# Kernel tuning notes

Measured on AMD Instinct MI355X. Metric: run time of the kernel, lower is better.

The kernel has to match this reference:

```python
import jax, jax.numpy as jnp
import numpy as np
import math

N_HEAD = 16  # from init_kwargs

def setup_inputs() -> dict:
    key = jax.random.key(0)
    ks = jax.random.split(key, 11)
    B, T, D = 2, 2048, 1024
    s = 0.02
    return {
        "q": jax.random.normal(ks[0], (B, T, D), jnp.float32),
        "k": jax.random.normal(ks[1], (B, T, D), jnp.float32),
        "v": jax.random.normal(ks[2], (B, T, D), jnp.float32),
        "Wq": jax.random.normal(ks[3], (D, D), jnp.float32) * s,
        "bq": jax.random.normal(ks[4], (D,), jnp.float32) * s,
        "Wk": jax.random.normal(ks[5], (D, D), jnp.float32) * s,
        "bk": jax.random.normal(ks[6], (D,), jnp.float32) * s,
        "Wv": jax.random.normal(ks[7], (D, D), jnp.float32) * s,
        "bv": jax.random.normal(ks[8], (D,), jnp.float32) * s,
        "Wc": jax.random.normal(ks[9], (D, D), jnp.float32) * s,
        "bc": jax.random.normal(ks[10], (D,), jnp.float32) * s,
    }

def reference(q, k, v, Wq, bq, Wk, bk, Wv, bv, Wc, bc):
    B, T, D = q.shape
    H = N_HEAD
    nd = D // H

    def proj(x, W, b):
        # torch Linear: x @ W.T + b; then split heads -> [b, h, t, nd]
        y = x @ W.T + b
        return y.reshape(B, T, H, nd).transpose(0, 2, 1, 3)

    qh = proj(q, Wq, bq)
    kh = proj(k, Wk, bk)
    vh = proj(v, Wv, bv)

    # scores: [b, h, t_q, t_k]
    z = jnp.einsum('bhqd,bhkd->bhqk', qh, kh) / math.sqrt(nd)
    mask = jnp.tril(jnp.ones((T, T), dtype=bool))  # causal
    z = jnp.where(mask, z, -jnp.inf)
    # NOTE: original uses nn.Softmax(dim=-2) -> softmax over the QUERY axis
    attn = jax.nn.softmax(z, axis=-2)
    out = jnp.einsum('bhqk,bhkd->bhqd', attn, vh)  # [b, h, t, nd]
    out = out.transpose(0, 2, 1, 3).reshape(B, T, D)
    return out @ Wc.T + bc
```

## Files before the change

kernel.cpp:

```cpp
#include <hip/hip_runtime.h>


#define Dd 1024
#define Tt 2048
#define Bb 2
#define Hh 16
#define NDh 64
#define Mm (Bb * Tt)

using u16 = unsigned short;
using u32 = unsigned int;
typedef __attribute__((ext_vector_type(8))) short bf16x8;
typedef __attribute__((ext_vector_type(4))) float f32x4;

__device__ __forceinline__ u16 f2bf(float f) {
  return (u16)((__float_as_uint(f) + 0x8000u) >> 16);
}
__device__ __forceinline__ u32 pk2(float a, float b) {
  u32 ua = __float_as_uint(a) + 0x8000u;
  u32 ub = __float_as_uint(b) + 0x8000u;
  return __builtin_amdgcn_perm(ub, ua, 0x07060302u);
}
__device__ __forceinline__ void ldsdma16(const u16* g, u16* l) {
  __builtin_amdgcn_global_load_lds(
      (const __attribute__((address_space(1))) u32*)g,
      (__attribute__((address_space(3))) u32*)l, 16, 0, 0);
}
#define MFMA(a, b, c) __builtin_amdgcn_mfma_f32_16x16x32_bf16((a), (b), (c), 0, 0, 0)

__global__ __launch_bounds__(256) void cvt_w(
    const float* __restrict__ w0, const float* __restrict__ w1,
    const float* __restrict__ w2, const float* __restrict__ w3,
    u16* __restrict__ dst)
{
  const int vid = blockIdx.x * 256 + threadIdx.x;
  const int seg = vid >> 18;
  const int off = (vid & 0x3FFFF) * 4;
  const float* s = seg == 0 ? w0 : seg == 1 ? w1 : seg == 2 ? w2 : w3;
  float4 f = *(const float4*)(s + off);
  ushort4 o;
  o.x = f2bf(f.x); o.y = f2bf(f.y); o.z = f2bf(f.z); o.w = f2bf(f.w);
  *(ushort4*)(dst + (size_t)seg * Dd * Dd + off) = o;
}

template <bool XF32>
__device__ __forceinline__ void gemm_body(
    const void* Xv, const u16* __restrict__ WB, const float* __restrict__ bias,
    void* Yv, float oscale, int omode, u16* As, u16* Bs)
{
  const int t = threadIdx.x, lane = t & 63, w = t >> 6;
  const int col = lane & 15, quad = lane >> 4;
  const int m0 = blockIdx.x * 64, n0 = blockIdx.y * 128;
  const int wm = (w >> 1) * 32, wn = (w & 1) * 64;
  const int drr = lane >> 3, dcc = (lane & 7) * 8;
  const int ar = t >> 2, ac = (t & 3) * 16;

  f32x4 acc[2][4] = {};
  float4 xf[4];
  const float* X32 = (const float*)Xv;
  if constexpr (XF32) {
#pragma unroll
    for (int j = 0; j < 4; j++)
      xf[j] = ((const float4*)(X32 + (size_t)(m0 + ar) * Dd + ac))[j];
  }

  for (int k0 = 0; k0 < Dd; k0 += 64) {
    __syncthreads();
#pragma unroll
    for (int i = 0; i < 4; i++) {
      const int rr = w * 32 + i * 8;
      ldsdma16(WB + (size_t)(n0 + rr + drr) * Dd + k0 + dcc, Bs + rr * 64);
    }
    if constexpr (XF32) {
      u32 pk[8];
#pragma unroll
      for (int j = 0; j < 4; j++) {
        pk[2 * j]     = pk2(xf[j].x, xf[j].y);
        pk[2 * j + 1] = pk2(xf[j].z, xf[j].w);
      }
      u16* dst = As + ar * 64 + ac;
      ((uint4*)dst)[0] = make_uint4(pk[0], pk[1], pk[2], pk[3]);
      ((uint4*)dst)[1] = make_uint4(pk[4], pk[5], pk[6], pk[7]);
      if (k0 + 64 < Dd) {
#pragma unroll
        for (int j = 0; j < 4; j++)
          xf[j] = ((const float4*)(X32 + (size_t)(m0 + ar) * Dd + k0 + 64 + ac))[j];
      }
    } else {
      const u16* X = (const u16*)Xv;
#pragma unroll
      for (int i = 0; i < 2; i++) {
        const int rr = w * 16 + i * 8;
        ldsdma16(X + (size_t)(m0 + rr + drr) * Dd + k0 + dcc, As + rr * 64);
      }
    }
    __syncthreads();
#pragma unroll
    for (int s = 0; s < 2; s++) {
      bf16x8 a[2], b[4];
#pragma unroll
      for (int i = 0; i < 2; i++)
        a[i] = *(const bf16x8*)(As + (wm + i * 16 + col) * 64 + s * 32 + quad * 8);
#pragma unroll
      for (int j = 0; j < 4; j++)
        b[j] = *(const bf16x8*)(Bs + (wn + j * 16 + col) * 64 + s * 32 + quad * 8);
#pragma unroll
      for (int i = 0; i < 2; i++)
#pragma unroll
        for (int j = 0; j < 4; j++)
          acc[i][j] = MFMA(a[i], b[j], acc[i][j]);
    }
  }

#pragma unroll
  for (int jt = 0; jt < 4; jt++) {
    const int n = n0 + wn + jt * 16 + col;
    const float bn = bias[n];
    if (omode == 1) {
#pragma unroll
      for (int i = 0; i < 2; i++) {
        const int mg = m0 + wm + i * 16 + quad * 4;
        const int bb = mg >> 11, tl = mg & 2047;
        ushort4 o;
        o.x = f2bf(acc[i][jt][0] + bn);
        o.y = f2bf(acc[i][jt][1] + bn);
        o.z = f2bf(acc[i][jt][2] + bn);
        o.w = f2bf(acc[i][jt][3] + bn);
        *(ushort4*)((u16*)Yv + (size_t)bb * Dd * Tt + (size_t)n * Tt + tl) = o;
      }
    } else if (omode == 0) {
      u16* Y = (u16*)Yv;
#pragma unroll
      for (int i = 0; i < 2; i++)
#pragma unroll
        for (int r = 0; r < 4; r++) {
          const int m = m0 + wm + i * 16 + quad * 4 + r;
          Y[(size_t)m * Dd + n] = f2bf((acc[i][jt][r] + bn) * oscale);
        }
    } else {
      float* Y = (float*)Yv;
#pragma unroll
      for (int i = 0; i < 2; i++)
#pragma unroll
        for (int r = 0; r < 4; r++) {
          const int m = m0 + wm + i * 16 + quad * 4 + r;
          Y[(size_t)m * Dd + n] = acc[i][jt][r] + bn;
        }
    }
  }
}

__global__ __launch_bounds__(256) void proj_qkv(
    const float* __restrict__ q, const float* __restrict__ k,
    const float* __restrict__ v, const u16* __restrict__ Wb,
    const float* __restrict__ bq, const float* __restrict__ bk,
    const float* __restrict__ bv,
    u16* __restrict__ Qp, u16* __restrict__ Kp, u16* __restrict__ VtG)
{
  __shared__ u16 As[64 * 64];
  __shared__ u16 Bs[128 * 64];
  const int z = blockIdx.z;
  const float* X = z == 0 ? q : z == 1 ? k : v;
  const u16* W = Wb + (size_t)z * Dd * Dd;
  const float* bias = z == 0 ? bq : z == 1 ? bk : bv;
  void* Y = z == 0 ? (void*)Qp : z == 1 ? (void*)Kp : (void*)VtG;
  gemm_body<true>(X, W, bias, Y, z == 0 ? 0.125f : 1.0f, z == 2 ? 1 : 0, As, Bs);
}

__global__ __launch_bounds__(256) void gemm_final(
    const u16* __restrict__ Ctx, const u16* __restrict__ Wcb,
    const float* __restrict__ bc, float* __restrict__ out)
{
  __shared__ u16 As[64 * 64];
  __shared__ u16 Bs[128 * 64];
  gemm_body<false>(Ctx, Wcb, bc, out, 1.0f, 2, As, Bs);
}

__global__ __launch_bounds__(256) void attn_stats(
    const u16* __restrict__ Qp, const u16* __restrict__ Kp,
    float* __restrict__ rlOut)
{
  __shared__ u16 Ks[128 * 64];
  __shared__ u16 Qs[64 * 64];
  const int t = threadIdx.x, lane = t & 63, w = t >> 6;
  const int col = lane & 15, quad = lane >> 4;
  const int bh = blockIdx.x, b = bh >> 4, h = bh & 15;
  const int tk0 = blockIdx.y * 128;
  const u16* Kbase = Kp + (size_t)b * Tt * Dd + h * NDh;
  const u16* Qbase = Qp + (size_t)b * Tt * Dd + h * NDh;
  const int drr = lane >> 3, dcc = (lane & 7) * 8;

#pragma unroll
  for (int i = 0; i < 4; i++) {
    const int rr = w * 32 + i * 8;
    ldsdma16(Kbase + (size_t)(tk0 + rr + drr) * Dd + dcc, Ks + rr * 64);
  }
  __syncthreads();
  bf16x8 ka[2][2];
#pragma unroll
  for (int s2 = 0; s2 < 2; s2++) {
    const int row = w * 32 + s2 * 16 + col;
    ka[s2][0] = *(const bf16x8*)(Ks + row * 64 + quad * 8);
    ka[s2][1] = *(const bf16x8*)(Ks + row * 64 + 32 + quad * 8);
  }

  float l[2][4] = {};

  auto tile = [&](int tq0, bool masked) {
    __syncthreads();
#pragma unroll
    for (int i = 0; i < 2; i++) {
      const int rr = w * 16 + i * 8;
      ldsdma16(Qbase + (size_t)(tq0 + rr + drr) * Dd + dcc, Qs + rr * 64);
    }
    __syncthreads();
#pragma unroll
    for (int jt = 0; jt < 4; jt++) {
      bf16x8 qb0 = *(const bf16x8*)(Qs + (jt * 16 + col) * 64 + quad * 8);
      bf16x8 qb1 = *(const bf16x8*)(Qs + (jt * 16 + col) * 64 + 32 + quad * 8);
      const int tq = tq0 + jt * 16 + col;
#pragma unroll
      for (int s2 = 0; s2 < 2; s2++) {
        f32x4 z = {};
        z = MFMA(ka[s2][0], qb0, z);
        z = MFMA(ka[s2][1], qb1, z);
#pragma unroll
        for (int r = 0; r < 4; r++) {
          float e = __expf(z[r]);
          if (masked) {
            const int tk = tk0 + w * 32 + s2 * 16 + quad * 4 + r;
            e = (tq >= tk) ? e : 0.f;
          }
          l[s2][r] += e;
        }
      }
    }
  };

  tile(tk0, true);
  tile(tk0 + 64, true);
  for (int tq0 = tk0 + 128; tq0 < Tt; tq0 += 64) tile(tq0, false);

#pragma unroll
  for (int s2 = 0; s2 < 2; s2++)
#pragma unroll
    for (int r = 0; r < 4; r++) {
      float s = l[s2][r];
#pragma unroll
      for (int m = 1; m < 16; m <<= 1) s += __shfl_xor(s, m);
      if (col == 0)
        rlOut[(size_t)bh * Tt + tk0 + w * 32 + s2 * 16 + quad * 4 + r] = 1.0f / s;
    }
}

__global__ __launch_bounds__(256) void attn_out(
    const u16* __restrict__ Qp, const u16* __restrict__ Kp,
    const u16* __restrict__ VtG, const float* __restrict__ rlIn,
    u16* __restrict__ Ctx)
{
  __shared__ u16 PQ[128 * 64];
  __shared__ u16 Ks[64 * 64];
  __shared__ u16 Vts[64 * 64];
  __shared__ float srl[64];
  const int t = threadIdx.x, lane = t & 63, w = t >> 6;
  const int col = lane & 15, quad = lane >> 4;
  const int bh = blockIdx.x, b = bh >> 4, h = bh & 15;
  const int tq0 = blockIdx.y * 128;
  const u16* Qbase = Qp + (size_t)b * Tt * Dd + h * NDh;
  const u16* Kbase = Kp + (size_t)b * Tt * Dd + h * NDh;
  const u16* Vbase = VtG + (size_t)b * Dd * Tt + (size_t)h * NDh * Tt;
  const int drr = lane >> 3, dcc = (lane & 7) * 8;

#pragma unroll
  for (int i = 0; i < 4; i++) {
    const int rr = w * 32 + i * 8;
    ldsdma16(Qbase + (size_t)(tq0 + rr + drr) * Dd + dcc, PQ + rr * 64);
  }
  __syncthreads();
  bf16x8 qa[2][2];
#pragma unroll
  for (int s2 = 0; s2 < 2; s2++) {
    const int row = w * 32 + s2 * 16 + col;
    qa[s2][0] = *(const bf16x8*)(PQ + row * 64 + quad * 8);
    qa[s2][1] = *(const bf16x8*)(PQ + row * 64 + 32 + quad * 8);
  }

  f32x4 o[2][4] = {};

  auto tile = [&](int tk0, bool masked) {
    __syncthreads();
#pragma unroll
    for (int i = 0; i < 2; i++) {
      const int rr = w * 16 + i * 8;
      ldsdma16(Kbase + (size_t)(tk0 + rr + drr) * Dd + dcc, Ks + rr * 64);
      ldsdma16(Vbase + (size_t)(rr + drr) * Tt + tk0 + dcc, Vts + rr * 64);
    }
    if (t < 64) srl[t] = rlIn[(size_t)bh * Tt + tk0 + t];
    __syncthreads();
#pragma unroll
    for (int jt = 0; jt < 4; jt++) {
      bf16x8 kb0 = *(const bf16x8*)(Ks + (jt * 16 + col) * 64 + quad * 8);
      bf16x8 kb1 = *(const bf16x8*)(Ks + (jt * 16 + col) * 64 + 32 + quad * 8);
      const int tkl = jt * 16 + col;
      const float rl = srl[tkl];
#pragma unroll
      for (int s2 = 0; s2 < 2; s2++) {
        f32x4 z = {};
        z = MFMA(qa[s2][0], kb0, z);
        z = MFMA(qa[s2][1], kb1, z);
#pragma unroll
        for (int r = 0; r < 4; r++) {
          float p = __expf(z[r]) * rl;
          if (masked) {
            const int tqg = tq0 + w * 32 + s2 * 16 + quad * 4 + r;
            p = (tk0 + tkl <= tqg) ? p : 0.f;
          }
          PQ[(w * 32 + s2 * 16 + quad * 4 + r) * 64 + tkl] = f2bf(p);
        }
      }
    }
    bf16x8 pa[2][2];
#pragma unroll
    for (int s2 = 0; s2 < 2; s2++) {
      const int row = w * 32 + s2 * 16 + col;
      pa[s2][0] = *(const bf16x8*)(PQ + row * 64 + quad * 8);
      pa[s2][1] = *(const bf16x8*)(PQ + row * 64 + 32 + quad * 8);
    }
#pragma unroll
    for (int dn = 0; dn < 4; dn++) {
      bf16x8 vb0 = *(const bf16x8*)(Vts + (dn * 16 + col) * 64 + quad * 8);
      bf16x8 vb1 = *(const bf16x8*)(Vts + (dn * 16 + col) * 64 + 32 + quad * 8);
#pragma unroll
      for (int s2 = 0; s2 < 2; s2++) {
        o[s2][dn] = MFMA(pa[s2][0], vb0, o[s2][dn]);
        o[s2][dn] = MFMA(pa[s2][1], vb1, o[s2][dn]);
      }
    }
  };

  for (int tk0 = 0; tk0 + 64 <= tq0; tk0 += 64) tile(tk0, false);
  tile(tq0, true);
  tile(tq0 + 64, true);

#pragma unroll
  for (int s2 = 0; s2 < 2; s2++)
#pragma unroll
    for (int dn = 0; dn < 4; dn++)
#pragma unroll
      for (int r = 0; r < 4; r++) {
        const int tq = tq0 + w * 32 + s2 * 16 + quad * 4 + r;
        Ctx[(size_t)(b * Tt + tq) * Dd + h * NDh + dn * 16 + col] = f2bf(o[s2][dn][r]);
      }
}

extern "C" void kernel_launch(void* const* d_in, const int* in_sizes, int n_in,
                              void* d_out, int out_size, void* d_ws, size_t ws_size,
                              hipStream_t stream)
{
  const float* q  = (const float*)d_in[0];
  const float* k  = (const float*)d_in[1];
  const float* v  = (const float*)d_in[2];
  const float* Wq = (const float*)d_in[3];
  const float* bq = (const float*)d_in[4];
  const float* Wk = (const float*)d_in[5];
  const float* bk = (const float*)d_in[6];
  const float* Wv = (const float*)d_in[7];
  const float* bv = (const float*)d_in[8];
  const float* Wc = (const float*)d_in[9];
  const float* bc = (const float*)d_in[10];

  u16* Wb  = (u16*)d_ws;
  u16* Qp  = Wb + (size_t)4 * Dd * Dd;
  u16* Kp  = Qp + (size_t)Mm * Dd;
  u16* VtG = Kp + (size_t)Mm * Dd;
  u16* Ctx = VtG + (size_t)Mm * Dd;
  float* rl = (float*)(Ctx + (size_t)Mm * Dd);

  cvt_w<<<4096, 256, 0, stream>>>(Wq, Wk, Wv, Wc, Wb);
  proj_qkv<<<dim3(Mm / 64, Dd / 128, 3), 256, 0, stream>>>(
      q, k, v, Wb, bq, bk, bv, Qp, Kp, VtG);
  attn_stats<<<dim3(Bb * Hh, Tt / 128), 256, 0, stream>>>(Qp, Kp, rl);
  attn_out<<<dim3(Bb * Hh, Tt / 128), 256, 0, stream>>>(Qp, Kp, VtG, rl, Ctx);
  gemm_final<<<dim3(Mm / 64, Dd / 128), 256, 0, stream>>>(
      Ctx, Wb + (size_t)3 * Dd * Dd, bc, (float*)d_out);
}
```

Before: 279.1 us.

## Swizzle LDS tiles, split attention stats and final GEMM with atomics, finer attn_out blocks

Applies an XOR swizzle to all LDS tile layouts to reduce bank conflicts on MFMA fragment reads. attn_stats is split four ways along the query axis and accumulates column sums with atomics. attn_out moves to 64-row query blocks scheduled heaviest-first to balance the causal workload. The final GEMM is split-K across two slices with atomic float adds into an output zeroed in cvt_w. Together these raise parallelism and occupancy, at the cost of atomic traffic and non-deterministic summation order.

```diff
diff --git a/kernel.cpp b/kernel.cpp
--- a/kernel.cpp
+++ b/kernel.cpp
@@ -27,11 +27,14 @@
       (__attribute__((address_space(3))) u32*)l, 16, 0, 0);
 }
 #define MFMA(a, b, c) __builtin_amdgcn_mfma_f32_16x16x32_bf16((a), (b), (c), 0, 0, 0)
+__device__ __forceinline__ bf16x8 ldfrag(const u16* lds, int row, int kgrp) {
+  return *(const bf16x8*)(lds + row * 64 + (((kgrp) ^ (row & 7)) * 8));
+}
 
 __global__ __launch_bounds__(256) void cvt_w(
     const float* __restrict__ w0, const float* __restrict__ w1,
     const float* __restrict__ w2, const float* __restrict__ w3,
-    u16* __restrict__ dst)
+    u16* __restrict__ dst, float* __restrict__ outz, float* __restrict__ lsumz)
 {
   const int vid = blockIdx.x * 256 + threadIdx.x;
   const int seg = vid >> 18;
@@ -41,19 +44,23 @@
   ushort4 o;
   o.x = f2bf(f.x); o.y = f2bf(f.y); o.z = f2bf(f.z); o.w = f2bf(f.w);
   *(ushort4*)(dst + (size_t)seg * Dd * Dd + off) = o;
+  *(float4*)(outz + (size_t)vid * 4) = make_float4(0.f, 0.f, 0.f, 0.f);
+  if (vid < Bb * Hh * Tt / 4)
+    *(float4*)(lsumz + (size_t)vid * 4) = make_float4(0.f, 0.f, 0.f, 0.f);
 }
 
 template <bool XF32>
 __device__ __forceinline__ void gemm_body(
     const void* Xv, const u16* __restrict__ WB, const float* __restrict__ bias,
-    void* Yv, float oscale, int omode, u16* As, u16* Bs)
+    void* Yv, float oscale, int omode, int kc, int knum, u16* As, u16* Bs)
 {
   const int t = threadIdx.x, lane = t & 63, w = t >> 6;
   const int col = lane & 15, quad = lane >> 4;
   const int m0 = blockIdx.x * 64, n0 = blockIdx.y * 128;
   const int wm = (w >> 1) * 32, wn = (w & 1) * 64;
-  const int drr = lane >> 3, dcc = (lane & 7) * 8;
-  const int ar = t >> 2, ac = (t & 3) * 16;
+  const int drr = lane >> 3, dsw = ((lane & 7) ^ drr) * 8;
+  const int ar = t >> 2, ag = (t & 3) * 2;
+  const int kbeg = (Dd / knum) * kc, kend = kbeg + Dd / knum;
 
   f32x4 acc[2][4] = {};
   float4 xf[4];
@@ -61,15 +68,15 @@
   if constexpr (XF32) {
 #pragma unroll
     for (int j = 0; j < 4; j++)
-      xf[j] = ((const float4*)(X32 + (size_t)(m0 + ar) * Dd + ac))[j];
-  }
-
-  for (int k0 = 0; k0 < Dd; k0 += 64) {
+      xf[j] = ((const float4*)(X32 + (size_t)(m0 + ar) * Dd + kbeg + ag * 8))[j];
+  }
+
+  for (int k0 = kbeg; k0 < kend; k0 += 64) {
     __syncthreads();
 #pragma unroll
     for (int i = 0; i < 4; i++) {
       const int rr = w * 32 + i * 8;
-      ldsdma16(WB + (size_t)(n0 + rr + drr) * Dd + k0 + dcc, Bs + rr * 64);
+      ldsdma16(WB + (size_t)(n0 + rr + drr) * Dd + k0 + dsw, Bs + rr * 64);
     }
     if constexpr (XF32) {
       u32 pk[8];
@@ -78,20 +85,20 @@
         pk[2 * j]     = pk2(xf[j].x, xf[j].y);
         pk[2 * j + 1] = pk2(xf[j].z, xf[j].w);
       }
-      u16* dst = As + ar * 64 + ac;
-      ((uint4*)dst)[0] = make_uint4(pk[0], pk[1], pk[2], pk[3]);
-      ((uint4*)dst)[1] = make_uint4(pk[4], pk[5], pk[6], pk[7]);
-      if (k0 + 64 < Dd) {
+      u16* dst = As + ar * 64;
+      *(uint4*)(dst + ((ag ^ (ar & 7)) * 8))       = make_uint4(pk[0], pk[1], pk[2], pk[3]);
+      *(uint4*)(dst + (((ag + 1) ^ (ar & 7)) * 8)) = make_uint4(pk[4], pk[5], pk[6], pk[7]);
+      if (k0 + 64 < kend) {
 #pragma unroll
         for (int j = 0; j < 4; j++)
-          xf[j] = ((const float4*)(X32 + (size_t)(m0 + ar) * Dd + k0 + 64 + ac))[j];
+          xf[j] = ((const float4*)(X32 + (size_t)(m0 + ar) * Dd + k0 + 64 + ag * 8))[j];
       }
     } else {
       const u16* X = (const u16*)Xv;
 #pragma unroll
       for (int i = 0; i < 2; i++) {
         const int rr = w * 16 + i * 8;
-        ldsdma16(X + (size_t)(m0 + rr + drr) * Dd + k0 + dcc, As + rr * 64);
+        ldsdma16(X + (size_t)(m0 + rr + drr) * Dd + k0 + dsw, As + rr * 64);
       }
     }
     __syncthreads();
@@ -100,10 +107,10 @@
       bf16x8 a[2], b[4];
 #pragma unroll
       for (int i = 0; i < 2; i++)
-        a[i] = *(const bf16x8*)(As + (wm + i * 16 + col) * 64 + s * 32 + quad * 8);
+        a[i] = ldfrag(As, wm + i * 16 + col, s * 4 + quad);
 #pragma unroll
       for (int j = 0; j < 4; j++)
-        b[j] = *(const bf16x8*)(Bs + (wn + j * 16 + col) * 64 + s * 32 + quad * 8);
+        b[j] = ldfrag(Bs, wn + j * 16 + col, s * 4 + quad);
 #pragma unroll
       for (int i = 0; i < 2; i++)
 #pragma unroll
@@ -115,7 +122,7 @@
 #pragma unroll
   for (int jt = 0; jt < 4; jt++) {
     const int n = n0 + wn + jt * 16 + col;
-    const float bn = bias[n];
+    const float bn = (omode == 2 && kc != 0) ? 0.f : bias[n];
     if (omode == 1) {
 #pragma unroll
       for (int i = 0; i < 2; i++) {
@@ -144,7 +151,7 @@
 #pragma unroll
         for (int r = 0; r < 4; r++) {
           const int m = m0 + wm + i * 16 + quad * 4 + r;
-          Y[(size_t)m * Dd + n] = acc[i][jt][r] + bn;
+          atomicAdd(&Y[(size_t)m * Dd + n], acc[i][jt][r] + bn);
         }
     }
   }
@@ -164,7 +171,7 @@
   const u16* W = Wb + (size_t)z * Dd * Dd;
   const float* bias = z == 0 ? bq : z == 1 ? bk : bv;
   void* Y = z == 0 ? (void*)Qp : z == 1 ? (void*)Kp : (void*)VtG;
-  gemm_body<true>(X, W, bias, Y, z == 0 ? 0.125f : 1.0f, z == 2 ? 1 : 0, As, Bs);
+  gemm_body<true>(X, W, bias, Y, z == 0 ? 0.125f : 1.0f, z == 2 ? 1 : 0, 0, 1, As, Bs);
 }
 
 __global__ __launch_bounds__(256) void gemm_final(
@@ -173,51 +180,53 @@
 {
   __shared__ u16 As[64 * 64];
   __shared__ u16 Bs[128 * 64];
-  gemm_body<false>(Ctx, Wcb, bc, out, 1.0f, 2, As, Bs);
+  gemm_body<false>(Ctx, Wcb, bc, out, 1.0f, 2, blockIdx.z, 2, As, Bs);
 }
 
 __global__ __launch_bounds__(256) void attn_stats(
     const u16* __restrict__ Qp, const u16* __restrict__ Kp,
-    float* __restrict__ rlOut)
+    float* __restrict__ lsum)
 {
   __shared__ u16 Ks[128 * 64];
   __shared__ u16 Qs[64 * 64];
   const int t = threadIdx.x, lane = t & 63, w = t >> 6;
   const int col = lane & 15, quad = lane >> 4;
   const int bh = blockIdx.x, b = bh >> 4, h = bh & 15;
-  const int tk0 = blockIdx.y * 128;
+  const int j = blockIdx.y, tk0 = j * 128, c = blockIdx.z;
   const u16* Kbase = Kp + (size_t)b * Tt * Dd + h * NDh;
   const u16* Qbase = Qp + (size_t)b * Tt * Dd + h * NDh;
-  const int drr = lane >> 3, dcc = (lane & 7) * 8;
+  const int drr = lane >> 3, dsw = ((lane & 7) ^ drr) * 8;
 
 #pragma unroll
   for (int i = 0; i < 4; i++) {
     const int rr = w * 32 + i * 8;
-    ldsdma16(Kbase + (size_t)(tk0 + rr + drr) * Dd + dcc, Ks + rr * 64);
+    ldsdma16(Kbase + (size_t)(tk0 + rr + drr) * Dd + dsw, Ks + rr * 64);
   }
   __syncthreads();
   bf16x8 ka[2][2];
 #pragma unroll
   for (int s2 = 0; s2 < 2; s2++) {
     const int row = w * 32 + s2 * 16 + col;
-    ka[s2][0] = *(const bf16x8*)(Ks + row * 64 + quad * 8);
-    ka[s2][1] = *(const bf16x8*)(Ks + row * 64 + 32 + quad * 8);
+    ka[s2][0] = ldfrag(Ks, row, quad);
+    ka[s2][1] = ldfrag(Ks, row, 4 + quad);
   }
 
   float l[2][4] = {};
 
-  auto tile = [&](int tq0, bool masked) {
+  for (int d = 2 * j + c, i0 = 0; d < Tt / 64; d += 4, i0++) {
+    const bool masked = (c < 2) && (i0 == 0);
+    const int tq0 = d * 64;
     __syncthreads();
 #pragma unroll
     for (int i = 0; i < 2; i++) {
       const int rr = w * 16 + i * 8;
-      ldsdma16(Qbase + (size_t)(tq0 + rr + drr) * Dd + dcc, Qs + rr * 64);
+      ldsdma16(Qbase + (size_t)(tq0 + rr + drr) * Dd + dsw, Qs + rr * 64);
     }
     __syncthreads();
 #pragma unroll
     for (int jt = 0; jt < 4; jt++) {
-      bf16x8 qb0 = *(const bf16x8*)(Qs + (jt * 16 + col) * 64 + quad * 8);
-      bf16x8 qb1 = *(const bf16x8*)(Qs + (jt * 16 + col) * 64 + 32 + quad * 8);
+      bf16x8 qb0 = ldfrag(Qs, jt * 16 + col, quad);
+      bf16x8 qb1 = ldfrag(Qs, jt * 16 + col, 4 + quad);
       const int tq = tq0 + jt * 16 + col;
 #pragma unroll
       for (int s2 = 0; s2 < 2; s2++) {
@@ -235,11 +244,7 @@
         }
       }
     }
-  };
-
-  tile(tk0, true);
-  tile(tk0 + 64, true);
-  for (int tq0 = tk0 + 128; tq0 < Tt; tq0 += 64) tile(tq0, false);
+  }
 
 #pragma unroll
   for (int s2 = 0; s2 < 2; s2++)
@@ -249,108 +254,86 @@
 #pragma unroll
       for (int m = 1; m < 16; m <<= 1) s += __shfl_xor(s, m);
       if (col == 0)
-        rlOut[(size_t)bh * Tt + tk0 + w * 32 + s2 * 16 + quad * 4 + r] = 1.0f / s;
+        atomicAdd(&lsum[(size_t)bh * Tt + tk0 + w * 32 + s2 * 16 + quad * 4 + r], s);
     }
 }
 
 __global__ __launch_bounds__(256) void attn_out(
     const u16* __restrict__ Qp, const u16* __restrict__ Kp,
-    const u16* __restrict__ VtG, const float* __restrict__ rlIn,
+    const u16* __restrict__ VtG, const float* __restrict__ lsum,
     u16* __restrict__ Ctx)
 {
-  __shared__ u16 PQ[128 * 64];
+  __shared__ u16 QPs[64 * 64];
   __shared__ u16 Ks[64 * 64];
   __shared__ u16 Vts[64 * 64];
   __shared__ float srl[64];
   const int t = threadIdx.x, lane = t & 63, w = t >> 6;
   const int col = lane & 15, quad = lane >> 4;
   const int bh = blockIdx.x, b = bh >> 4, h = bh & 15;
-  const int tq0 = blockIdx.y * 128;
+  const int tq0 = (gridDim.y - 1 - blockIdx.y) * 64;
   const u16* Qbase = Qp + (size_t)b * Tt * Dd + h * NDh;
   const u16* Kbase = Kp + (size_t)b * Tt * Dd + h * NDh;
   const u16* Vbase = VtG + (size_t)b * Dd * Tt + (size_t)h * NDh * Tt;
-  const int drr = lane >> 3, dcc = (lane & 7) * 8;
-
-#pragma unroll
-  for (int i = 0; i < 4; i++) {
-    const int rr = w * 32 + i * 8;
-    ldsdma16(Qbase + (size_t)(tq0 + rr + drr) * Dd + dcc, PQ + rr * 64);
+  const int drr = lane >> 3, dsw = ((lane & 7) ^ drr) * 8;
+
+#pragma unroll
+  for (int i = 0; i < 2; i++) {
+    const int rr = w * 16 + i * 8;
+    ldsdma16(Qbase + (size_t)(tq0 + rr + drr) * Dd + dsw, QPs + rr * 64);
   }
   __syncthreads();
-  bf16x8 qa[2][2];
-#pragma unroll
-  for (int s2 = 0; s2 < 2; s2++) {
-    const int row = w * 32 + s2 * 16 + col;
-    qa[s2][0] = *(const bf16x8*)(PQ + row * 64 + quad * 8);
-    qa[s2][1] = *(const bf16x8*)(PQ + row * 64 + 32 + quad * 8);
-  }
-
-  f32x4 o[2][4] = {};
-
-  auto tile = [&](int tk0, bool masked) {
+  bf16x8 qa[2];
+  qa[0] = ldfrag(QPs, w * 16 + col, quad);
+  qa[1] = ldfrag(QPs, w * 16 + col, 4 + quad);
+
+  f32x4 o[4] = {};
+
+  for (int tk0 = 0; tk0 <= tq0; tk0 += 64) {
+    const bool masked = (tk0 == tq0);
     __syncthreads();
 #pragma unroll
     for (int i = 0; i < 2; i++) {
       const int rr = w * 16 + i * 8;
-      ldsdma16(Kbase + (size_t)(tk0 + rr + drr) * Dd + dcc, Ks + rr * 64);
-      ldsdma16(Vbase + (size_t)(rr + drr) * Tt + tk0 + dcc, Vts + rr * 64);
-    }
-    if (t < 64) srl[t] = rlIn[(size_t)bh * Tt + tk0 + t];
+      ldsdma16(Kbase + (size_t)(tk0 + rr + drr) * Dd + dsw, Ks + rr * 64);
+      ldsdma16(Vbase + (size_t)(rr + drr) * Tt + tk0 + dsw, Vts + rr * 64);
+    }
+    if (t < 64) srl[t] = 1.0f / lsum[(size_t)bh * Tt + tk0 + t];
     __syncthreads();
 #pragma unroll
     for (int jt = 0; jt < 4; jt++) {
-      bf16x8 kb0 = *(const bf16x8*)(Ks + (jt * 16 + col) * 64 + quad * 8);
-      bf16x8 kb1 = *(const bf16x8*)(Ks + (jt * 16 + col) * 64 + 32 + quad * 8);
+      bf16x8 kb0 = ldfrag(Ks, jt * 16 + col, quad);
+      bf16x8 kb1 = ldfrag(Ks, jt * 16 + col, 4 + quad);
       const int tkl = jt * 16 + col;
       const float rl = srl[tkl];
-#pragma unroll
-      for (int s2 = 0; s2 < 2; s2++) {
-        f32x4 z = {};
-        z = MFMA(qa[s2][0], kb0, z);
-        z = MFMA(qa[s2][1], kb1, z);
-#pragma unroll
-        for (int r = 0; r < 4; r++) {
-          float p = __expf(z[r]) * rl;
-          if (masked) {
-            const int tqg = tq0 + w * 32 + s2 * 16 + quad * 4 + r;
-            p = (tk0 + tkl <= tqg) ? p : 0.f;
-          }
-          PQ[(w * 32 + s2 * 16 + quad * 4 + r) * 64 + tkl] = f2bf(p);
-        }
-      }
-    }
-    bf16x8 pa[2][2];
-#pragma unroll
-    for (int s2 = 0; s2 < 2; s2++) {
-      const int row = w * 32 + s2 * 16 + col;
-      pa[s2][0] = *(const bf16x8*)(PQ + row * 64 + quad * 8);
-      pa[s2][1] = *(const bf16x8*)(PQ + row * 64 + 32 + quad * 8);
-    }
+      f32x4 z = {};
+      z = MFMA(qa[0], kb0, z);
+      z = MFMA(qa[1], kb1, z);
+#pragma unroll
+      for (int r = 0; r < 4; r++) {
+        const int row = w * 16 + quad * 4 + r;
+        float p = __expf(z[r]) * rl;
+        if (masked) p = (tkl <= row) ? p : 0.f;
+        QPs[row * 64 + (((tkl >> 3) ^ (row & 7)) * 8) + (tkl & 7)] = f2bf(p);
+      }
+    }
+    bf16x8 pa0 = ldfrag(QPs, w * 16 + col, quad);
+    bf16x8 pa1 = ldfrag(QPs, w * 16 + col, 4 + quad);
 #pragma unroll
     for (int dn = 0; dn < 4; dn++) {
-      bf16x8 vb0 = *(const bf16x8*)(Vts + (dn * 16 + col) * 64 + quad * 8);
-      bf16x8 vb1 = *(const bf16x8*)(Vts + (dn * 16 + col) * 64 + 32 + quad * 8);
-#pragma unroll
-      for (int s2 = 0; s2 < 2; s2++) {
-        o[s2][dn] = MFMA(pa[s2][0], vb0, o[s2][dn]);
-        o[s2][dn] = MFMA(pa[s2][1], vb1, o[s2][dn]);
-      }
-    }
-  };
-
-  for (int tk0 = 0; tk0 + 64 <= tq0; tk0 += 64) tile(tk0, false);
-  tile(tq0, true);
-  tile(tq0 + 64, true);
-
-#pragma unroll
-  for (int s2 = 0; s2 < 2; s2++)
-#pragma unroll
-    for (int dn = 0; dn < 4; dn++)
-#pragma unroll
-      for (int r = 0; r < 4; r++) {
-        const int tq = tq0 + w * 32 + s2 * 16 + quad * 4 + r;
-        Ctx[(size_t)(b * Tt + tq) * Dd + h * NDh + dn * 16 + col] = f2bf(o[s2][dn][r]);
-      }
+      bf16x8 vb0 = ldfrag(Vts, dn * 16 + col, quad);
+      bf16x8 vb1 = ldfrag(Vts, dn * 16 + col, 4 + quad);
+      o[dn] = MFMA(pa0, vb0, o[dn]);
+      o[dn] = MFMA(pa1, vb1, o[dn]);
+    }
+  }
+
+#pragma unroll
+  for (int dn = 0; dn < 4; dn++)
+#pragma unroll
+    for (int r = 0; r < 4; r++) {
+      const int tq = tq0 + w * 16 + quad * 4 + r;
+      Ctx[(size_t)(b * Tt + tq) * Dd + h * NDh + dn * 16 + col] = f2bf(o[dn][r]);
+    }
 }
 
 extern "C" void kernel_launch(void* const* d_in, const int* in_sizes, int n_in,
@@ -369,18 +352,18 @@
   const float* Wc = (const float*)d_in[9];
   const float* bc = (const float*)d_in[10];
 
-  u16* Wb  = (u16*)d_ws;
-  u16* Qp  = Wb + (size_t)4 * Dd * Dd;
-  u16* Kp  = Qp + (size_t)Mm * Dd;
-  u16* VtG = Kp + (size_t)Mm * Dd;
-  u16* Ctx = VtG + (size_t)Mm * Dd;
-  float* rl = (float*)(Ctx + (size_t)Mm * Dd);
-
-  cvt_w<<<4096, 256, 0, stream>>>(Wq, Wk, Wv, Wc, Wb);
+  u16* Wb   = (u16*)d_ws;
+  u16* Qp   = Wb + (size_t)4 * Dd * Dd;
+  u16* Kp   = Qp + (size_t)Mm * Dd;
+  u16* VtG  = Kp + (size_t)Mm * Dd;
+  u16* Ctx  = VtG + (size_t)Mm * Dd;
+  float* lsum = (float*)(Ctx + (size_t)Mm * Dd);
+
+  cvt_w<<<4096, 256, 0, stream>>>(Wq, Wk, Wv, Wc, Wb, (float*)d_out, lsum);
   proj_qkv<<<dim3(Mm / 64, Dd / 128, 3), 256, 0, stream>>>(
       q, k, v, Wb, bq, bk, bv, Qp, Kp, VtG);
-  attn_stats<<<dim3(Bb * Hh, Tt / 128), 256, 0, stream>>>(Qp, Kp, rl);
-  attn_out<<<dim3(Bb * Hh, Tt / 128), 256, 0, stream>>>(Qp, Kp, VtG, rl, Ctx);
-  gemm_final<<<dim3(Mm / 64, Dd / 128), 256, 0, stream>>>(
+  attn_stats<<<dim3(Bb * Hh, Tt / 128, 4), 256, 0, stream>>>(Qp, Kp, lsum);
+  attn_out<<<dim3(Bb * Hh, Tt / 64), 256, 0, stream>>>(Qp, Kp, VtG, lsum, Ctx);
+  gemm_final<<<dim3(Mm / 64, Dd / 128, 2), 256, 0, stream>>>(
       Ctx, Wb + (size_t)3 * Dd * Dd, bc, (float*)d_out);
 }
```

Result: faster. 268.8 us (-3.7%).
